# Kernel optimization log

Measured on AMD Instinct MI355X. Metric: run time of the kernel, lower is better.

Reference implementation:

```python
import jax, jax.numpy as jnp
import numpy as np

D_MODEL = 1024
N_HEADS = 16
HEAD_DIM = D_MODEL // N_HEADS
B, S = 4, 2048


def setup_inputs() -> dict:
    key = jax.random.key(0)
    ks = jax.random.split(key, 5)
    scale = 1.0 / np.sqrt(D_MODEL)
    return {
        "x": jax.random.normal(ks[0], (B, S, D_MODEL), dtype=jnp.float32),
        "w_q": jax.random.normal(ks[1], (D_MODEL, D_MODEL), dtype=jnp.float32) * scale,
        "w_k": jax.random.normal(ks[2], (D_MODEL, D_MODEL), dtype=jnp.float32) * scale,
        "w_v": jax.random.normal(ks[3], (D_MODEL, D_MODEL), dtype=jnp.float32) * scale,
        "w_o": jax.random.normal(ks[4], (D_MODEL, D_MODEL), dtype=jnp.float32) * scale,
    }


def _split_heads(t):
    # [b, s, d_model] -> [b, h, s, head_dim]
    b, s, _ = t.shape
    return t.reshape(b, s, N_HEADS, HEAD_DIM).transpose(0, 2, 1, 3)


def reference(x, w_q, w_k, w_v, w_o):
    b, s, _ = x.shape
    # bias-free linears: y = x @ W^T (weight is [out, in])
    q = _split_heads(jnp.einsum('bsd,ed->bse', x, w_q))
    k = _split_heads(jnp.einsum('bsd,ed->bse', x, w_k))
    v = _split_heads(jnp.einsum('bsd,ed->bse', x, w_v))
    scores = jnp.einsum('bhqd,bhkd->bhqk', q, k) / jnp.sqrt(
        jnp.asarray(HEAD_DIM, dtype=x.dtype))
    causal = jnp.tril(jnp.ones((s, s), dtype=bool))  # [s, s]
    scores = jnp.where(causal[None, None], scores, -jnp.inf)
    probs = jax.nn.softmax(scores, axis=-1)
    out = jnp.einsum('bhqk,bhkd->bhqd', probs, v)
    out = out.transpose(0, 2, 1, 3).reshape(b, s, D_MODEL)  # merge heads
    return jnp.einsum('bsd,ed->bse', out, w_o)
```

## Files before the change

kernel.cpp:

```cpp
#include <hip/hip_runtime.h>
#include <hip/hip_bf16.h>
#include <stdint.h>


typedef __bf16 bf16_t;
typedef bf16_t bf16x8 __attribute__((ext_vector_type(8)));
typedef bf16_t bf16x4 __attribute__((ext_vector_type(4)));
typedef float f32x4 __attribute__((ext_vector_type(4)));

static __device__ __forceinline__ void gload_lds16(const void* g, void* l) {
  __builtin_amdgcn_global_load_lds((const __attribute__((address_space(1))) void*)g,
                                   (__attribute__((address_space(3))) void*)l,
                                   16, 0, 0);
}

__global__ __launch_bounds__(256) void cvt_f32_bf16(const float* __restrict__ src,
                                                    bf16_t* __restrict__ dst, int n4) {
  int i = blockIdx.x * blockDim.x + threadIdx.x;
  if (i >= n4) return;
  float4 v = reinterpret_cast<const float4*>(src)[i];
  bf16x4 o;
  o[0] = (bf16_t)v.x; o[1] = (bf16_t)v.y; o[2] = (bf16_t)v.z; o[3] = (bf16_t)v.w;
  reinterpret_cast<bf16x4*>(dst)[i] = o;
}

__global__ __launch_bounds__(256) void cvt_w4(const float* __restrict__ w0, const float* __restrict__ w1,
                                              const float* __restrict__ w2, const float* __restrict__ w3,
                                              bf16_t* __restrict__ o0, bf16_t* __restrict__ o1,
                                              bf16_t* __restrict__ o2, bf16_t* __restrict__ o3, int n4) {
  const float* s; bf16_t* d;
  switch (blockIdx.y) {
    case 0: s = w0; d = o0; break;
    case 1: s = w1; d = o1; break;
    case 2: s = w2; d = o2; break;
    default: s = w3; d = o3; break;
  }
  int i = blockIdx.x * blockDim.x + threadIdx.x;
  if (i >= n4) return;
  float4 v = reinterpret_cast<const float4*>(s)[i];
  bf16x4 o;
  o[0] = (bf16_t)v.x; o[1] = (bf16_t)v.y; o[2] = (bf16_t)v.z; o[3] = (bf16_t)v.w;
  reinterpret_cast<bf16x4*>(d)[i] = o;
}

__global__ __launch_bounds__(256) void gemm_bt(const bf16_t* __restrict__ A,
                                               const bf16_t* __restrict__ W,
                                               void* __restrict__ Cout,
                                               int mode, float scale) {
  const int K = 1024;
  __shared__ __align__(16) bf16_t sA[128 * 64];
  __shared__ __align__(16) bf16_t sB[128 * 64];
  const int tid = threadIdx.x;
  const int wave = tid >> 6, lane = tid & 63;
  const int lr = lane & 15, hi = lane >> 4;
  const int bm = blockIdx.y, bn = blockIdx.x;
  const bf16_t* Ab = A + (size_t)bm * 128 * K;
  const bf16_t* Wb = W + (size_t)bn * 128 * K;
  const int wr = (wave >> 1) * 64, wc = (wave & 1) * 64;

  f32x4 acc[4][4] = {};

  const int srow = tid >> 3;
  const int scol = (tid & 7) << 3;

  for (int kt = 0; kt < K / 64; ++kt) {
    const int k0 = kt * 64;
#pragma unroll
    for (int i = 0; i < 4; ++i) {
      gload_lds16(Ab + (size_t)(i * 32 + srow) * K + k0 + scol, sA + i * 2048 + wave * 512);
      gload_lds16(Wb + (size_t)(i * 32 + srow) * K + k0 + scol, sB + i * 2048 + wave * 512);
    }
    __syncthreads();
#pragma unroll
    for (int kk = 0; kk < 2; ++kk) {
      bf16x8 af[4], bfr[4];
#pragma unroll
      for (int m = 0; m < 4; ++m)
        af[m] = *reinterpret_cast<const bf16x8*>(&sA[(wr + m * 16 + lr) * 64 + kk * 32 + hi * 8]);
#pragma unroll
      for (int n = 0; n < 4; ++n)
        bfr[n] = *reinterpret_cast<const bf16x8*>(&sB[(wc + n * 16 + lr) * 64 + kk * 32 + hi * 8]);
#pragma unroll
      for (int m = 0; m < 4; ++m)
#pragma unroll
        for (int n = 0; n < 4; ++n)
          acc[m][n] = __builtin_amdgcn_mfma_f32_16x16x32_bf16(af[m], bfr[n], acc[m][n], 0, 0, 0);
    }
    __syncthreads();
  }

  const int row0 = bm * 128 + wr;
  const int col0 = bn * 128 + wc;
  if (mode == 3) {
    float* C = (float*)Cout;
#pragma unroll
    for (int m = 0; m < 4; ++m)
#pragma unroll
      for (int n = 0; n < 4; ++n)
#pragma unroll
        for (int j = 0; j < 4; ++j)
          C[(size_t)(row0 + m * 16 + hi * 4 + j) * 1024 + col0 + n * 16 + lr] = acc[m][n][j];
  } else if (mode == 2) {
    bf16_t* C = (bf16_t*)Cout;
#pragma unroll
    for (int m = 0; m < 4; ++m)
#pragma unroll
      for (int n = 0; n < 4; ++n)
#pragma unroll
        for (int j = 0; j < 4; ++j) {
          int i = row0 + m * 16 + hi * 4 + j;
          int e = col0 + n * 16 + lr;
          int b = i >> 11, s = i & 2047, h = e >> 6, dh = e & 63;
          C[((size_t)((b * 16 + h) * 64 + dh)) * 2048 + s] = (bf16_t)acc[m][n][j];
        }
  } else {
    bf16_t* C = (bf16_t*)Cout;
#pragma unroll
    for (int m = 0; m < 4; ++m)
#pragma unroll
      for (int n = 0; n < 4; ++n)
#pragma unroll
        for (int j = 0; j < 4; ++j) {
          int i = row0 + m * 16 + hi * 4 + j;
          int e = col0 + n * 16 + lr;
          int b = i >> 11, s = i & 2047, h = e >> 6, dh = e & 63;
          C[((size_t)((b * 16 + h) * 2048 + s)) * 64 + dh] = (bf16_t)(acc[m][n][j] * scale);
        }
  }
}

__global__ __launch_bounds__(256) void attn_causal(const bf16_t* __restrict__ Q,
                                                   const bf16_t* __restrict__ Kb,
                                                   const bf16_t* __restrict__ Vt,
                                                   bf16_t* __restrict__ O) {
  __shared__ __align__(16) bf16_t sK[2][64 * 64];
  __shared__ __align__(16) bf16_t sV[2][64 * 64];
  __shared__ __align__(16) bf16_t sP[4][16 * 72];
  const int bid = blockIdx.x;
  const int slot = bid >> 3;
  const int bh = (bid & 7) * 8 + (slot >> 4);
  const int pair = slot & 15;
  const int qt_lo = pair, qt_hi = 31 - pair;
  const int tid = threadIdx.x, wave = tid >> 6, lane = tid & 63;
  const int lr = lane & 15, hi = lane >> 4;
  const bf16_t* Qp = Q + (size_t)bh * 2048 * 64;
  const char* Kg = (const char*)(Kb + (size_t)bh * 2048 * 64);
  const char* Vg = (const char*)(Vt + (size_t)bh * 64 * 2048);

  const int q0_lo = qt_lo * 64 + wave * 16;
  const int q0_hi = qt_hi * 64 + wave * 16;

  bf16x8 qfl[2], qfh[2];
  qfl[0] = *reinterpret_cast<const bf16x8*>(&Qp[(size_t)(q0_lo + lr) * 64 + hi * 8]);
  qfl[1] = *reinterpret_cast<const bf16x8*>(&Qp[(size_t)(q0_lo + lr) * 64 + 32 + hi * 8]);
  qfh[0] = *reinterpret_cast<const bf16x8*>(&Qp[(size_t)(q0_hi + lr) * 64 + hi * 8]);
  qfh[1] = *reinterpret_cast<const bf16x8*>(&Qp[(size_t)(q0_hi + lr) * 64 + 32 + hi * 8]);

  bf16x8 ones;
#pragma unroll
  for (int i = 0; i < 8; ++i) ones[i] = (bf16_t)1.0f;

  f32x4 o_lo[4] = {}, o_hi[4] = {};
  f32x4 lacc_lo = {}, lacc_hi = {};

  const float EXPC = 17.312340490667562f;

  auto stage = [&](int t, int buf) {
#pragma unroll
    for (int c = 0; c < 2; ++c) {
      const int L = c * 4096 + wave * 1024 + (lane << 4);
      const int row = L >> 7;
      const int swz = (row & 7) << 4;
      gload_lds16(Kg + (size_t)t * 8192 + (size_t)(L ^ swz),
                  (char*)sK[buf] + c * 4096 + wave * 1024);
      gload_lds16(Vg + (size_t)row * 4096 + (size_t)t * 128 + (size_t)((L & 127) ^ swz),
                  (char*)sV[buf] + c * 4096 + wave * 1024);
    }
  };

  auto do_tile = [&](int buf, const bf16x8* qf, f32x4* oacc, f32x4& lacc,
                     int q0, bool domask, int t) {
    f32x4 s[4] = {};
#pragma unroll
    for (int kk = 0; kk < 2; ++kk) {
#pragma unroll
      for (int n = 0; n < 4; ++n) {
        const int r = n * 16 + lr;
        const int cb = (kk * 64 + hi * 16) ^ ((r & 7) << 4);
        bf16x8 kf = *reinterpret_cast<const bf16x8*>((const char*)sK[buf] + r * 128 + cb);
        s[n] = __builtin_amdgcn_mfma_f32_16x16x32_bf16(qf[kk], kf, s[n], 0, 0, 0);
      }
    }
    if (domask) {
#pragma unroll
      for (int n = 0; n < 4; ++n)
#pragma unroll
        for (int j = 0; j < 4; ++j)
          if (t * 64 + n * 16 + lr > q0 + hi * 4 + j) s[n][j] = -INFINITY;
    }
#pragma unroll
    for (int n = 0; n < 4; ++n)
#pragma unroll
      for (int j = 0; j < 4; ++j)
        sP[wave][(hi * 4 + j) * 72 + n * 16 + lr] = (bf16_t)exp2f(s[n][j] - EXPC);
#pragma unroll
    for (int kk = 0; kk < 2; ++kk) {
      bf16x8 pf = *reinterpret_cast<const bf16x8*>(&sP[wave][lr * 72 + kk * 32 + hi * 8]);
      lacc = __builtin_amdgcn_mfma_f32_16x16x32_bf16(pf, ones, lacc, 0, 0, 0);
#pragma unroll
      for (int n = 0; n < 4; ++n) {
        const int r = n * 16 + lr;
        const int cb = (kk * 64 + hi * 16) ^ ((r & 7) << 4);
        bf16x8 vf = *reinterpret_cast<const bf16x8*>((const char*)sV[buf] + r * 128 + cb);
        oacc[n] = __builtin_amdgcn_mfma_f32_16x16x32_bf16(pf, vf, oacc[n], 0, 0, 0);
      }
    }
  };

  stage(0, 0);
  int cur = 0;
  for (int t = 0; t <= qt_hi; ++t) {
    __syncthreads();
    if (t < qt_hi) stage(t + 1, cur ^ 1);
    do_tile(cur, qfh, o_hi, lacc_hi, q0_hi, t == qt_hi, t);
    if (t <= qt_lo) do_tile(cur, qfl, o_lo, lacc_lo, q0_lo, t == qt_lo, t);
    cur ^= 1;
  }

  const int b = bh >> 4, h = bh & 15;
#pragma unroll
  for (int n = 0; n < 4; ++n)
#pragma unroll
    for (int j = 0; j < 4; ++j) {
      const int ql = q0_lo + hi * 4 + j;
      const int qh = q0_hi + hi * 4 + j;
      O[(size_t)(b * 2048 + ql) * 1024 + h * 64 + n * 16 + lr] = (bf16_t)(o_lo[n][j] / lacc_lo[j]);
      O[(size_t)(b * 2048 + qh) * 1024 + h * 64 + n * 16 + lr] = (bf16_t)(o_hi[n][j] / lacc_hi[j]);
    }
}

extern "C" void kernel_launch(void* const* d_in, const int* in_sizes, int n_in,
                              void* d_out, int out_size, void* d_ws, size_t ws_size,
                              hipStream_t stream) {
  const float* x  = (const float*)d_in[0];
  const float* wq = (const float*)d_in[1];
  const float* wk = (const float*)d_in[2];
  const float* wv = (const float*)d_in[3];
  const float* wo = (const float*)d_in[4];

  char* ws = (char*)d_ws;
  bf16_t* xb  = (bf16_t*)(ws);
  bf16_t* wqb = (bf16_t*)(ws + (16ull << 20));
  bf16_t* wkb = (bf16_t*)(ws + (18ull << 20));
  bf16_t* wvb = (bf16_t*)(ws + (20ull << 20));
  bf16_t* wob = (bf16_t*)(ws + (22ull << 20));
  bf16_t* Qb  = (bf16_t*)(ws + (24ull << 20));
  bf16_t* Kbf = (bf16_t*)(ws + (40ull << 20));
  bf16_t* Vtb = (bf16_t*)(ws + (56ull << 20));
  bf16_t* Ob  = (bf16_t*)(ws + (72ull << 20));

  cvt_f32_bf16<<<8192, 256, 0, stream>>>(x, xb, 2097152);
  cvt_w4<<<dim3(1024, 4), 256, 0, stream>>>(wq, wk, wv, wo, wqb, wkb, wvb, wob, 262144);

  dim3 gg(8, 64);
  gemm_bt<<<gg, 256, 0, stream>>>(xb, wqb, Qb, 0, 0.18033688011112042f);
  gemm_bt<<<gg, 256, 0, stream>>>(xb, wkb, Kbf, 1, 1.0f);
  gemm_bt<<<gg, 256, 0, stream>>>(xb, wvb, Vtb, 2, 1.0f);

  attn_causal<<<1024, 256, 0, stream>>>(Qb, Kbf, Vtb, Ob);

  gemm_bt<<<gg, 256, 0, stream>>>(Ob, wob, d_out, 3, 1.0f);
}
```

Baseline: 301.2 us.

## Merge QKV GEMMs into one launch and split attention to one q-tile per block

The three Q/K/V projection GEMMs are combined into a single launch that selects the weight and output layout from blockIdx.z. The attention kernel stops pairing a low and a high query tile per block and launches 2048 blocks with one tile each, ordered heaviest first, with a launch-bounds occupancy hint. V is no longer staged in LDS: each wave reads V fragments directly from global memory in the PV loop, which frees shared memory but adds uncached-pattern global loads per tile. The score accumulator starts at the negative constant, so the exp offset subtraction drops out.

```diff
diff --git a/kernel.cpp b/kernel.cpp
--- a/kernel.cpp
+++ b/kernel.cpp
@@ -43,10 +43,92 @@
   reinterpret_cast<bf16x4*>(d)[i] = o;
 }
 
+__global__ __launch_bounds__(256) void gemm_qkv(const bf16_t* __restrict__ A,
+                                                const bf16_t* __restrict__ w0,
+                                                const bf16_t* __restrict__ w1,
+                                                const bf16_t* __restrict__ w2,
+                                                bf16_t* __restrict__ c0,
+                                                bf16_t* __restrict__ c1,
+                                                bf16_t* __restrict__ c2,
+                                                float qscale) {
+  const int K = 1024;
+  __shared__ __align__(16) bf16_t sA[128 * 64];
+  __shared__ __align__(16) bf16_t sB[128 * 64];
+  const int z = blockIdx.z;
+  const bf16_t* W = (z == 0) ? w0 : (z == 1 ? w1 : w2);
+  const int tid = threadIdx.x;
+  const int wave = tid >> 6, lane = tid & 63;
+  const int lr = lane & 15, hi = lane >> 4;
+  const int bm = blockIdx.y, bn = blockIdx.x;
+  const bf16_t* Ab = A + (size_t)bm * 128 * K;
+  const bf16_t* Wb = W + (size_t)bn * 128 * K;
+  const int wr = (wave >> 1) * 64, wc = (wave & 1) * 64;
+
+  f32x4 acc[4][4] = {};
+  const int srow = tid >> 3;
+  const int scol = (tid & 7) << 3;
+
+  for (int kt = 0; kt < K / 64; ++kt) {
+    const int k0 = kt * 64;
+#pragma unroll
+    for (int i = 0; i < 4; ++i) {
+      gload_lds16(Ab + (size_t)(i * 32 + srow) * K + k0 + scol, sA + i * 2048 + wave * 512);
+      gload_lds16(Wb + (size_t)(i * 32 + srow) * K + k0 + scol, sB + i * 2048 + wave * 512);
+    }
+    __syncthreads();
+#pragma unroll
+    for (int kk = 0; kk < 2; ++kk) {
+      bf16x8 af[4], bfr[4];
+#pragma unroll
+      for (int m = 0; m < 4; ++m)
+        af[m] = *reinterpret_cast<const bf16x8*>(&sA[(wr + m * 16 + lr) * 64 + kk * 32 + hi * 8]);
+#pragma unroll
+      for (int n = 0; n < 4; ++n)
+        bfr[n] = *reinterpret_cast<const bf16x8*>(&sB[(wc + n * 16 + lr) * 64 + kk * 32 + hi * 8]);
+#pragma unroll
+      for (int m = 0; m < 4; ++m)
+#pragma unroll
+        for (int n = 0; n < 4; ++n)
+          acc[m][n] = __builtin_amdgcn_mfma_f32_16x16x32_bf16(af[m], bfr[n], acc[m][n], 0, 0, 0);
+    }
+    __syncthreads();
+  }
+
+  const int row0 = bm * 128 + wr;
+  const int col0 = bn * 128 + wc;
+  if (z == 2) {
+    bf16_t* C = c2;
+#pragma unroll
+    for (int m = 0; m < 4; ++m)
+#pragma unroll
+      for (int n = 0; n < 4; ++n)
+#pragma unroll
+        for (int j = 0; j < 4; ++j) {
+          int i = row0 + m * 16 + hi * 4 + j;
+          int e = col0 + n * 16 + lr;
+          int b = i >> 11, s = i & 2047, h = e >> 6, dh = e & 63;
+          C[((size_t)((b * 16 + h) * 64 + dh)) * 2048 + s] = (bf16_t)acc[m][n][j];
+        }
+  } else {
+    bf16_t* C = (z == 0) ? c0 : c1;
+    const float scale = (z == 0) ? qscale : 1.0f;
+#pragma unroll
+    for (int m = 0; m < 4; ++m)
+#pragma unroll
+      for (int n = 0; n < 4; ++n)
+#pragma unroll
+        for (int j = 0; j < 4; ++j) {
+          int i = row0 + m * 16 + hi * 4 + j;
+          int e = col0 + n * 16 + lr;
+          int b = i >> 11, s = i & 2047, h = e >> 6, dh = e & 63;
+          C[((size_t)((b * 16 + h) * 2048 + s)) * 64 + dh] = (bf16_t)(acc[m][n][j] * scale);
+        }
+  }
+}
+
 __global__ __launch_bounds__(256) void gemm_bt(const bf16_t* __restrict__ A,
                                                const bf16_t* __restrict__ W,
-                                               void* __restrict__ Cout,
-                                               int mode, float scale) {
+                                               float* __restrict__ C) {
   const int K = 1024;
   __shared__ __align__(16) bf16_t sA[128 * 64];
   __shared__ __align__(16) bf16_t sB[128 * 64];
@@ -59,7 +141,6 @@
   const int wr = (wave >> 1) * 64, wc = (wave & 1) * 64;
 
   f32x4 acc[4][4] = {};
-
   const int srow = tid >> 3;
   const int scol = (tid & 7) << 3;
 
@@ -91,79 +172,45 @@
 
   const int row0 = bm * 128 + wr;
   const int col0 = bn * 128 + wc;
-  if (mode == 3) {
-    float* C = (float*)Cout;
-#pragma unroll
-    for (int m = 0; m < 4; ++m)
-#pragma unroll
-      for (int n = 0; n < 4; ++n)
-#pragma unroll
-        for (int j = 0; j < 4; ++j)
-          C[(size_t)(row0 + m * 16 + hi * 4 + j) * 1024 + col0 + n * 16 + lr] = acc[m][n][j];
-  } else if (mode == 2) {
-    bf16_t* C = (bf16_t*)Cout;
-#pragma unroll
-    for (int m = 0; m < 4; ++m)
-#pragma unroll
-      for (int n = 0; n < 4; ++n)
-#pragma unroll
-        for (int j = 0; j < 4; ++j) {
-          int i = row0 + m * 16 + hi * 4 + j;
-          int e = col0 + n * 16 + lr;
-          int b = i >> 11, s = i & 2047, h = e >> 6, dh = e & 63;
-          C[((size_t)((b * 16 + h) * 64 + dh)) * 2048 + s] = (bf16_t)acc[m][n][j];
-        }
-  } else {
-    bf16_t* C = (bf16_t*)Cout;
-#pragma unroll
-    for (int m = 0; m < 4; ++m)
-#pragma unroll
-      for (int n = 0; n < 4; ++n)
-#pragma unroll
-        for (int j = 0; j < 4; ++j) {
-          int i = row0 + m * 16 + hi * 4 + j;
-          int e = col0 + n * 16 + lr;
-          int b = i >> 11, s = i & 2047, h = e >> 6, dh = e & 63;
-          C[((size_t)((b * 16 + h) * 2048 + s)) * 64 + dh] = (bf16_t)(acc[m][n][j] * scale);
-        }
-  }
-}
-
-__global__ __launch_bounds__(256) void attn_causal(const bf16_t* __restrict__ Q,
-                                                   const bf16_t* __restrict__ Kb,
-                                                   const bf16_t* __restrict__ Vt,
-                                                   bf16_t* __restrict__ O) {
+#pragma unroll
+  for (int m = 0; m < 4; ++m)
+#pragma unroll
+    for (int n = 0; n < 4; ++n)
+#pragma unroll
+      for (int j = 0; j < 4; ++j)
+        C[(size_t)(row0 + m * 16 + hi * 4 + j) * 1024 + col0 + n * 16 + lr] = acc[m][n][j];
+}
+
+__global__ __launch_bounds__(256, 4) void attn_causal(const bf16_t* __restrict__ Q,
+                                                      const bf16_t* __restrict__ Kb,
+                                                      const bf16_t* __restrict__ Vt,
+                                                      bf16_t* __restrict__ O) {
   __shared__ __align__(16) bf16_t sK[2][64 * 64];
-  __shared__ __align__(16) bf16_t sV[2][64 * 64];
   __shared__ __align__(16) bf16_t sP[4][16 * 72];
   const int bid = blockIdx.x;
   const int slot = bid >> 3;
-  const int bh = (bid & 7) * 8 + (slot >> 4);
-  const int pair = slot & 15;
-  const int qt_lo = pair, qt_hi = 31 - pair;
+  const int bh = (bid & 7) * 8 + (slot >> 5);
+  const int qt = 31 - (slot & 31);
   const int tid = threadIdx.x, wave = tid >> 6, lane = tid & 63;
   const int lr = lane & 15, hi = lane >> 4;
   const bf16_t* Qp = Q + (size_t)bh * 2048 * 64;
   const char* Kg = (const char*)(Kb + (size_t)bh * 2048 * 64);
   const char* Vg = (const char*)(Vt + (size_t)bh * 64 * 2048);
 
-  const int q0_lo = qt_lo * 64 + wave * 16;
-  const int q0_hi = qt_hi * 64 + wave * 16;
-
-  bf16x8 qfl[2], qfh[2];
-  qfl[0] = *reinterpret_cast<const bf16x8*>(&Qp[(size_t)(q0_lo + lr) * 64 + hi * 8]);
-  qfl[1] = *reinterpret_cast<const bf16x8*>(&Qp[(size_t)(q0_lo + lr) * 64 + 32 + hi * 8]);
-  qfh[0] = *reinterpret_cast<const bf16x8*>(&Qp[(size_t)(q0_hi + lr) * 64 + hi * 8]);
-  qfh[1] = *reinterpret_cast<const bf16x8*>(&Qp[(size_t)(q0_hi + lr) * 64 + 32 + hi * 8]);
+  const int q0 = qt * 64 + wave * 16;
+
+  bf16x8 qf[2];
+  qf[0] = *reinterpret_cast<const bf16x8*>(&Qp[(size_t)(q0 + lr) * 64 + hi * 8]);
+  qf[1] = *reinterpret_cast<const bf16x8*>(&Qp[(size_t)(q0 + lr) * 64 + 32 + hi * 8]);
 
   bf16x8 ones;
 #pragma unroll
   for (int i = 0; i < 8; ++i) ones[i] = (bf16_t)1.0f;
 
-  f32x4 o_lo[4] = {}, o_hi[4] = {};
-  f32x4 lacc_lo = {}, lacc_hi = {};
-
-  const float EXPC = 17.312340490667562f;
+  f32x4 oacc[4] = {};
+  f32x4 lacc = {};
+
+  const float NEGC = -17.312340490667562f;
 
   auto stage = [&](int t, int buf) {
 #pragma unroll
@@ -173,25 +220,29 @@
       const int swz = (row & 7) << 4;
       gload_lds16(Kg + (size_t)t * 8192 + (size_t)(L ^ swz),
                   (char*)sK[buf] + c * 4096 + wave * 1024);
-      gload_lds16(Vg + (size_t)row * 4096 + (size_t)t * 128 + (size_t)((L & 127) ^ swz),
-                  (char*)sV[buf] + c * 4096 + wave * 1024);
     }
   };
 
-  auto do_tile = [&](int buf, const bf16x8* qf, f32x4* oacc, f32x4& lacc,
-                     int q0, bool domask, int t) {
-    f32x4 s[4] = {};
+  stage(0, 0);
+  int cur = 0;
+  for (int t = 0; t <= qt; ++t) {
+    __syncthreads();
+    if (t < qt) stage(t + 1, cur ^ 1);
+
+    f32x4 s[4];
+#pragma unroll
+    for (int n = 0; n < 4; ++n) { s[n][0] = NEGC; s[n][1] = NEGC; s[n][2] = NEGC; s[n][3] = NEGC; }
 #pragma unroll
     for (int kk = 0; kk < 2; ++kk) {
 #pragma unroll
       for (int n = 0; n < 4; ++n) {
         const int r = n * 16 + lr;
         const int cb = (kk * 64 + hi * 16) ^ ((r & 7) << 4);
-        bf16x8 kf = *reinterpret_cast<const bf16x8*>((const char*)sK[buf] + r * 128 + cb);
+        bf16x8 kf = *reinterpret_cast<const bf16x8*>((const char*)sK[cur] + r * 128 + cb);
         s[n] = __builtin_amdgcn_mfma_f32_16x16x32_bf16(qf[kk], kf, s[n], 0, 0, 0);
       }
     }
-    if (domask) {
+    if (t == qt) {
 #pragma unroll
       for (int n = 0; n < 4; ++n)
 #pragma unroll
@@ -202,28 +253,20 @@
     for (int n = 0; n < 4; ++n)
 #pragma unroll
       for (int j = 0; j < 4; ++j)
-        sP[wave][(hi * 4 + j) * 72 + n * 16 + lr] = (bf16_t)exp2f(s[n][j] - EXPC);
+        sP[wave][(hi * 4 + j) * 72 + n * 16 + lr] = (bf16_t)exp2f(s[n][j]);
 #pragma unroll
     for (int kk = 0; kk < 2; ++kk) {
+      bf16x8 vf[4];
+#pragma unroll
+      for (int n = 0; n < 4; ++n)
+        vf[n] = *reinterpret_cast<const bf16x8*>(
+            Vg + (size_t)(n * 16 + lr) * 4096 + (size_t)t * 128 + kk * 64 + hi * 16);
       bf16x8 pf = *reinterpret_cast<const bf16x8*>(&sP[wave][lr * 72 + kk * 32 + hi * 8]);
       lacc = __builtin_amdgcn_mfma_f32_16x16x32_bf16(pf, ones, lacc, 0, 0, 0);
 #pragma unroll
-      for (int n = 0; n < 4; ++n) {
-        const int r = n * 16 + lr;
-        const int cb = (kk * 64 + hi * 16) ^ ((r & 7) << 4);
-        bf16x8 vf = *reinterpret_cast<const bf16x8*>((const char*)sV[buf] + r * 128 + cb);
-        oacc[n] = __builtin_amdgcn_mfma_f32_16x16x32_bf16(pf, vf, oacc[n], 0, 0, 0);
-      }
-    }
-  };
-
-  stage(0, 0);
-  int cur = 0;
-  for (int t = 0; t <= qt_hi; ++t) {
-    __syncthreads();
-    if (t < qt_hi) stage(t + 1, cur ^ 1);
-    do_tile(cur, qfh, o_hi, lacc_hi, q0_hi, t == qt_hi, t);
-    if (t <= qt_lo) do_tile(cur, qfl, o_lo, lacc_lo, q0_lo, t == qt_lo, t);
+      for (int n = 0; n < 4; ++n)
+        oacc[n] = __builtin_amdgcn_mfma_f32_16x16x32_bf16(pf, vf[n], oacc[n], 0, 0, 0);
+    }
     cur ^= 1;
   }
 
@@ -232,10 +275,8 @@
   for (int n = 0; n < 4; ++n)
 #pragma unroll
     for (int j = 0; j < 4; ++j) {
-      const int ql = q0_lo + hi * 4 + j;
-      const int qh = q0_hi + hi * 4 + j;
-      O[(size_t)(b * 2048 + ql) * 1024 + h * 64 + n * 16 + lr] = (bf16_t)(o_lo[n][j] / lacc_lo[j]);
-      O[(size_t)(b * 2048 + qh) * 1024 + h * 64 + n * 16 + lr] = (bf16_t)(o_hi[n][j] / lacc_hi[j]);
+      const int q = q0 + hi * 4 + j;
+      O[(size_t)(b * 2048 + q) * 1024 + h * 64 + n * 16 + lr] = (bf16_t)(oacc[n][j] / lacc[j]);
     }
 }
 
@@ -262,12 +303,10 @@
   cvt_f32_bf16<<<8192, 256, 0, stream>>>(x, xb, 2097152);
   cvt_w4<<<dim3(1024, 4), 256, 0, stream>>>(wq, wk, wv, wo, wqb, wkb, wvb, wob, 262144);
 
-  dim3 gg(8, 64);
-  gemm_bt<<<gg, 256, 0, stream>>>(xb, wqb, Qb, 0, 0.18033688011112042f);
-  gemm_bt<<<gg, 256, 0, stream>>>(xb, wkb, Kbf, 1, 1.0f);
-  gemm_bt<<<gg, 256, 0, stream>>>(xb, wvb, Vtb, 2, 1.0f);
-
-  attn_causal<<<1024, 256, 0, stream>>>(Qb, Kbf, Vtb, Ob);
-
-  gemm_bt<<<gg, 256, 0, stream>>>(Ob, wob, d_out, 3, 1.0f);
-}
+  gemm_qkv<<<dim3(8, 64, 3), 256, 0, stream>>>(xb, wqb, wkb, wvb, Qb, Kbf, Vtb,
+                                               0.18033688011112042f);
+
+  attn_causal<<<2048, 256, 0, stream>>>(Qb, Kbf, Vtb, Ob);
+
+  gemm_bt<<<dim3(8, 64), 256, 0, stream>>>(Ob, wob, (float*)d_out);
+}
```

Measured after the change: 385.9 us. +28.1%, slower.
